# Performance work log

Hardware: AMD Instinct MI355X
Metric: run time of the kernel (lower is better)

## Reference

```python
import jax, jax.numpy as jnp
import numpy as np
import math

D = 256
H = 128
GATE_IN = 2 * D + 1 + 1 + 3  # mu, logvar, s, minutes, snr(3) = 517


def setup_inputs() -> dict:
    key = jax.random.key(0)
    ks = jax.random.split(key, 10)
    B, S = 256, 512
    mu = jax.random.normal(ks[0], (B, S, D), dtype=jnp.float32)
    logvar = jax.random.normal(ks[1], (B, S, D), dtype=jnp.float32)
    minutes = jax.random.uniform(ks[2], (B, S), dtype=jnp.float32) * 120.0
    mu_c = jax.random.normal(ks[3], (2, D), dtype=jnp.float32) * 0.1
    log_tau2 = jax.random.normal(ks[4], (2, D), dtype=jnp.float32) * 0.1
    log_prior = jax.random.normal(ks[5], (2,), dtype=jnp.float32) * 0.1
    W1 = jax.random.normal(ks[6], (H, GATE_IN), dtype=jnp.float32) * 0.05
    b1 = jnp.zeros((H,), dtype=jnp.float32)
    W2 = jax.random.normal(ks[7], (1, H), dtype=jnp.float32) * 0.05
    b2 = jnp.zeros((1,), dtype=jnp.float32)
    alpha_logits = jnp.float32(0.0)          # logit(0.5)
    attn_lambda_logit = jnp.float32(0.0)     # logit(0.5)
    decay_rate_log = jnp.float32(math.log(0.1))
    return dict(mu=mu, logvar=logvar, minutes=minutes, mu_c=mu_c,
                log_tau2=log_tau2, log_prior=log_prior, W1=W1, b1=b1,
                W2=W2, b2=b2, alpha_logits=alpha_logits,
                attn_lambda_logit=attn_lambda_logit,
                decay_rate_log=decay_rate_log)


def _logit(p):
    return jnp.log(p) - jnp.log1p(-p)


def reference(mu, logvar, minutes, mu_c, log_tau2, log_prior,
              W1, b1, W2, b2, alpha_logits, attn_lambda_logit,
              decay_rate_log):
    var = jnp.exp(logvar)                              # [B,S,D]

    def ell(c):
        tau2 = jnp.exp(log_tau2[c])                    # [D]
        diff2 = (mu - mu_c[c]) ** 2
        return -0.5 * jnp.sum((var + diff2) / tau2 + log_tau2[c], axis=-1)

    s = (ell(1) + log_prior[1]) - (ell(0) + log_prior[0])   # [B,S]

    # SNR features
    var_c = jnp.clip(var, 1e-6, None)
    snr1 = jnp.linalg.norm(mu, axis=-1) / math.sqrt(mu.shape[-1])
    snr2 = jnp.mean(logvar, axis=-1)
    snr3 = jnp.mean(mu ** 2 / var_c, axis=-1)
    snr = jnp.stack([snr1, snr2, snr3], axis=-1)            # [B,S,3]

    gate_in = jnp.concatenate(
        [mu, logvar, s[..., None], minutes[..., None], snr], axis=-1)

    h = jax.nn.relu(jnp.einsum('bsf,hf->bsh', gate_in, W1) + b1)
    a_raw = jax.nn.sigmoid(jnp.einsum('bsh,oh->bso', h, W2) + b2)[..., 0]

    # precision attention mixture
    score = jnp.sum(mu ** 2 / var_c, axis=-1)               # [B,S]
    a_prec = jax.nn.softmax(score, axis=1)
    a_mlp = a_raw / jnp.clip(jnp.sum(a_raw, axis=1, keepdims=True), 1e-6, None)
    lam = jax.nn.sigmoid(attn_lambda_logit)
    a = lam * a_mlp + (1.0 - lam) * a_prec

    # time decay
    last_time = jnp.max(minutes, axis=1, keepdims=True)
    delta_h = jnp.clip(last_time - minutes, 0.0, None) / 60.0
    rate = jax.nn.softplus(decay_rate_log)
    w = a * jnp.exp(-rate * delta_h)
    a = w / jnp.clip(jnp.sum(w, axis=1, keepdims=True), 1e-6, None)

    # mean aggregator
    s_main = jnp.sum(a * s, axis=1)                         # [B]

    # Noisy-OR branch
    p_i = jnp.clip(jax.nn.sigmoid(s) * a, 1e-6, 1.0 - 1e-6)
    log1m = jnp.sum(jnp.log1p(-p_i), axis=1)
    p_or = 1.0 - jnp.exp(log1m)
    s_or = _logit(jnp.clip(p_or, 1e-6, 1.0 - 1e-6))

    alpha = jax.nn.sigmoid(alpha_logits)
    s_total = alpha * s_main + (1.0 - alpha) * s_or
    return (s_total, s, a)
```

## Files before the change

### kernel.cpp

```cpp
#include <hip/hip_runtime.h>
#include <hip/hip_bf16.h>

#define B_DIM 256
#define NTOK (256 * 512)
#define W1_LD 517
#define TPB 32

#define WS_DIT 0
#define WS_E 256
#define WS_C0 512
#define WS_W1F 1024
#define WS_SCORE 36864

typedef __attribute__((ext_vector_type(8))) short bf16x8;
typedef __attribute__((ext_vector_type(4))) float f32x4;

__device__ __forceinline__ unsigned pk2(float a, float b) {
  __hip_bfloat162 h = __float22bfloat162_rn(make_float2(a, b));
  unsigned r;
  __builtin_memcpy(&r, &h, 4);
  return r;
}

template <int CTRL>
__device__ __forceinline__ float dpp_add(float v) {
  int s = __builtin_amdgcn_update_dpp(0, __float_as_int(v), CTRL, 0xf, 0xf,
                                      true);
  return v + __int_as_float(s);
}
__device__ __forceinline__ float row8_sum(float v) {
  v = dpp_add<0xB1>(v);
  v = dpp_add<0x4E>(v);
  v = dpp_add<0x141>(v);
  return v;
}
__device__ __forceinline__ float row16_sum(float v) {
  v = dpp_add<0xB1>(v);
  v = dpp_add<0x4E>(v);
  v = dpp_add<0x124>(v);
  v = dpp_add<0x128>(v);
  return v;
}

__device__ __forceinline__ float wave_sum(float v) {
#pragma unroll
  for (int off = 32; off > 0; off >>= 1) v += __shfl_xor(v, off, 64);
  return v;
}
__device__ __forceinline__ float wave_max(float v) {
#pragma unroll
  for (int off = 32; off > 0; off >>= 1) v = fmaxf(v, __shfl_xor(v, off, 64));
  return v;
}
__device__ __forceinline__ float block_sum(float v, float* scr) {
  v = wave_sum(v);
  int wid = threadIdx.x >> 6;
  __syncthreads();
  if ((threadIdx.x & 63) == 0) scr[wid] = v;
  __syncthreads();
  return scr[0] + scr[1] + scr[2] + scr[3];
}

__global__ __launch_bounds__(256) void k_setup(
    const float* __restrict__ W1, const float* __restrict__ b1,
    const float* __restrict__ mu_c, const float* __restrict__ log_tau2,
    const float* __restrict__ log_prior, float* __restrict__ wsc) {
  const int tid = threadIdx.x;
  const int h = blockIdx.x;
  ushort* w1f = (ushort*)(wsc + WS_W1F);
  const float* wr = W1 + h * W1_LD;
  const int k = 2 * tid;
  const unsigned pk = pk2(wr[k], wr[k + 1]);
  const int flat = (h >> 4) * 8704 + (k >> 5) * 512 +
                   (((k >> 3) & 3) * 16 + (h & 15)) * 8 + (k & 7);
  *(unsigned*)(w1f + flat) = pk;
  if (tid == 0) {
    const int base16 = (h >> 4) * 8704 + 16 * 512;
    uint4 g0;
    g0.x = pk2(wr[512], wr[513]);
    g0.y = pk2(wr[514], wr[515]);
    g0.z = pk2(wr[516], b1[h]);
    g0.w = 0u;
    *(uint4*)(w1f + base16 + ((h & 15)) * 8) = g0;
    const uint4 z = {0u, 0u, 0u, 0u};
    *(uint4*)(w1f + base16 + (16 + (h & 15)) * 8) = z;
    *(uint4*)(w1f + base16 + (32 + (h & 15)) * 8) = z;
    *(uint4*)(w1f + base16 + (48 + (h & 15)) * 8) = z;
  }

  if (blockIdx.x == 0) {
    __shared__ float scr[4];
    float lt0 = log_tau2[tid], lt1 = log_tau2[256 + tid];
    float mc0 = mu_c[tid], mc1 = mu_c[256 + tid];
    float it0 = __expf(-lt0), it1 = __expf(-lt1);
    wsc[WS_DIT + tid] = it1 - it0;
    wsc[WS_E + tid] = 2.0f * (mc1 * it1 - mc0 * it0);
    float g = mc1 * mc1 * it1 - mc0 * mc0 * it0 + (lt1 - lt0);
    float sg = block_sum(g, scr);
    if (tid == 0) wsc[WS_C0] = (log_prior[1] - log_prior[0]) - 0.5f * sg;
  }
}

__global__ __launch_bounds__(256, 4) void k_token(
    const float* __restrict__ mu, const float* __restrict__ logvar,
    const float* __restrict__ minutes, const float* __restrict__ W2g,
    const float* __restrict__ b2, const float* __restrict__ wsc,
    float* __restrict__ out_s, float* __restrict__ ws_score,
    float* __restrict__ araw_out) {
  __shared__ __align__(16) ushort A_l[TPB * 512];
  __shared__ __align__(16) ushort axl[TPB * 32];
  __shared__ float red2[4][TPB];

  const int tid = threadIdx.x;
  const int w = tid >> 6;
  const int l = tid & 63;
  const int tokbase = blockIdx.x * TPB;
  const float C0 = wsc[WS_C0];

  if (tid < 96) {
    const int row = tid & 31;
    const int c = tid >> 5;
    const uint4 z = {0u, 0u, 0u, 0u};
    *(uint4*)((char*)axl + row * 64 + 16 + c * 16) = z;
  }

  const int trow = tid >> 3;
  const int l8 = tid & 7;
  const int swz = (trow & 7) << 4;
  char* Ab = (char*)A_l;
  const size_t gbase = (size_t)(tokbase + trow) * 256 + l8 * 8;
  const float* ditg = wsc + WS_DIT + l8 * 8;
  const float* eg = wsc + WS_E + l8 * 8;
  float Ss = 0.f, Sm = 0.f, Sl = 0.f, Sc = 0.f;
#pragma unroll
  for (int t = 0; t < 4; ++t) {
    const float4 m0 = *(const float4*)(mu + gbase + t * 64);
    const float4 m1 = *(const float4*)(mu + gbase + t * 64 + 4);
    const float4 v0 = *(const float4*)(logvar + gbase + t * 64);
    const float4 v1 = *(const float4*)(logvar + gbase + t * 64 + 4);
    const float4 dA = *(const float4*)(ditg + t * 64);
    const float4 dB = *(const float4*)(ditg + t * 64 + 4);
    const float4 eA = *(const float4*)(eg + t * 64);
    const float4 eB = *(const float4*)(eg + t * 64 + 4);
#define CHUNK(m, lv, dt, ee)                                              \
  {                                                                       \
    const float va = __expf(lv.x), vb = __expf(lv.y), vc = __expf(lv.z),  \
                vd = __expf(lv.w);                                        \
    const float na = __expf(-lv.x), nb = __expf(-lv.y),                   \
                nc = __expf(-lv.z), nd = __expf(-lv.w);                   \
    const float qa = m.x * m.x, qb = m.y * m.y, qc = m.z * m.z,           \
                qd = m.w * m.w;                                           \
    Ss += (va + qa) * dt.x - m.x * ee.x + (vb + qb) * dt.y - m.y * ee.y + \
          (vc + qc) * dt.z - m.z * ee.z + (vd + qd) * dt.w - m.w * ee.w;  \
    Sm += qa + qb + qc + qd;                                              \
    Sl += lv.x + lv.y + lv.z + lv.w;                                      \
    Sc += qa * na + qb * nb + qc * nc + qd * nd;                          \
  }
    CHUNK(m0, v0, dA, eA);
    CHUNK(m1, v1, dB, eB);
#undef CHUNK
    uint4 um, uv;
    um.x = pk2(m0.x, m0.y);
    um.y = pk2(m0.z, m0.w);
    um.z = pk2(m1.x, m1.y);
    um.w = pk2(m1.z, m1.w);
    uv.x = pk2(v0.x, v0.y);
    uv.y = pk2(v0.z, v0.w);
    uv.z = pk2(v1.x, v1.y);
    uv.w = pk2(v1.z, v1.w);
    const int off = trow * 1024 + t * 128 + l8 * 16;
    *(uint4*)(Ab + (off ^ swz)) = um;
    *(uint4*)(Ab + ((off + 512) ^ swz)) = uv;
  }
  Ss = row8_sum(Ss);
  Sm = row8_sum(Sm);
  Sl = row8_sum(Sl);
  Sc = row8_sum(Sc);
  if (l8 == 0) {
    const float sval = -0.5f * Ss + C0;
    const float mn = minutes[tokbase + trow];
    uint4 ex;
    ex.x = pk2(sval, mn);
    ex.y = pk2(sqrtf(Sm) * (1.0f / 16.0f), Sl * (1.0f / 256.0f));
    ex.z = pk2(Sc * (1.0f / 256.0f), 1.0f);
    ex.w = 0u;
    *(uint4*)((char*)axl + trow * 64) = ex;
    out_s[tokbase + trow] = sval;
    ws_score[tokbase + trow] = Sc;
  }
  __syncthreads();

  f32x4 a00 = {0.f, 0.f, 0.f, 0.f};
  f32x4 a01 = {0.f, 0.f, 0.f, 0.f};
  f32x4 a10 = {0.f, 0.f, 0.f, 0.f};
  f32x4 a11 = {0.f, 0.f, 0.f, 0.f};
  const int m_lane = l & 15;
  const int swzA = (m_lane & 7) << 4;
  const int rowA0 = m_lane * 1024;
  const int rowA1 = rowA0 + 16 * 1024;
  const ushort* w1f = (const ushort*)(wsc + WS_W1F);
  const ushort* bp0 = w1f + (2 * w) * 8704 + l * 8;
  const ushort* bp1 = bp0 + 8704;
#pragma unroll 4
  for (int ks = 0; ks < 16; ++ks) {
    const int kByte = ks * 64 + (l >> 4) * 16;
    bf16x8 f0 = *(const bf16x8*)(Ab + ((rowA0 + kByte) ^ swzA));
    bf16x8 f1 = *(const bf16x8*)(Ab + ((rowA1 + kByte) ^ swzA));
    bf16x8 bq0 = *(const bf16x8*)(bp0 + ks * 512);
    bf16x8 bq1 = *(const bf16x8*)(bp1 + ks * 512);
    a00 = __builtin_amdgcn_mfma_f32_16x16x32_bf16(f0, bq0, a00, 0, 0, 0);
    a01 = __builtin_amdgcn_mfma_f32_16x16x32_bf16(f0, bq1, a01, 0, 0, 0);
    a10 = __builtin_amdgcn_mfma_f32_16x16x32_bf16(f1, bq0, a10, 0, 0, 0);
    a11 = __builtin_amdgcn_mfma_f32_16x16x32_bf16(f1, bq1, a11, 0, 0, 0);
  }
  {
    const int xb = (l >> 4) * 16;
    bf16x8 f0 = *(const bf16x8*)((char*)axl + m_lane * 64 + xb);
    bf16x8 f1 = *(const bf16x8*)((char*)axl + (m_lane + 16) * 64 + xb);
    bf16x8 bq0 = *(const bf16x8*)(bp0 + 16 * 512);
    bf16x8 bq1 = *(const bf16x8*)(bp1 + 16 * 512);
    a00 = __builtin_amdgcn_mfma_f32_16x16x32_bf16(f0, bq0, a00, 0, 0, 0);
    a01 = __builtin_amdgcn_mfma_f32_16x16x32_bf16(f0, bq1, a01, 0, 0, 0);
    a10 = __builtin_amdgcn_mfma_f32_16x16x32_bf16(f1, bq0, a10, 0, 0, 0);
    a11 = __builtin_amdgcn_mfma_f32_16x16x32_bf16(f1, bq1, a11, 0, 0, 0);
  }

  const int g = l >> 4;
  const float w2a = W2g[32 * w + m_lane];
  const float w2b = W2g[32 * w + m_lane + 16];
#pragma unroll
  for (int mf = 0; mf < 2; ++mf) {
    const f32x4 aN0 = mf ? a10 : a00;
    const f32x4 aN1 = mf ? a11 : a01;
#pragma unroll
    for (int r = 0; r < 4; ++r) {
      const int t_loc = 16 * mf + 4 * g + r;
      float cs = fmaxf(aN0[r], 0.f) * w2a + fmaxf(aN1[r], 0.f) * w2b;
      cs = row16_sum(cs);
      if (m_lane == 0) red2[w][t_loc] = cs;
    }
  }
  __syncthreads();
  if (tid < TPB) {
    float z = red2[0][tid] + red2[1][tid] + red2[2][tid] + red2[3][tid] +
              b2[0];
    araw_out[tokbase + tid] = 1.0f / (1.0f + __expf(-z));
  }
}

__global__ __launch_bounds__(256) void k_row(
    const float* __restrict__ minutes, const float* __restrict__ s_in,
    const float* __restrict__ score_in, float* a_io,
    const float* __restrict__ alpha_logits,
    const float* __restrict__ attn_lambda_logit,
    const float* __restrict__ decay_rate_log, float* __restrict__ out_total) {
  __shared__ float scrA[4][4];
  __shared__ float scrB[4];
  __shared__ float scrC[4];
  __shared__ float scrD[4][2];
  const int row = blockIdx.x;
  const int tid = threadIdx.x;
  const int w = tid >> 6;
  const int base = row * 512;
  const float sc0 = score_in[base + tid], sc1 = score_in[base + 256 + tid];
  const float sv0 = s_in[base + tid], sv1 = s_in[base + 256 + tid];
  const float ar0 = a_io[base + tid], ar1 = a_io[base + 256 + tid];
  const float mn0 = minutes[base + tid], mn1 = minutes[base + 256 + tid];

  const float vsc = wave_max(fmaxf(sc0, sc1));
  const float vmn = wave_max(fmaxf(mn0, mn1));
  const float var_ = wave_sum(ar0 + ar1);
  if ((tid & 63) == 0) {
    scrA[w][0] = vsc;
    scrA[w][1] = vmn;
    scrA[w][2] = var_;
  }
  __syncthreads();
  const float msc = fmaxf(fmaxf(scrA[0][0], scrA[1][0]),
                          fmaxf(scrA[2][0], scrA[3][0]));
  const float mmn = fmaxf(fmaxf(scrA[0][1], scrA[1][1]),
                          fmaxf(scrA[2][1], scrA[3][1]));
  const float sar = scrA[0][2] + scrA[1][2] + scrA[2][2] + scrA[3][2];

  const float e0 = __expf(sc0 - msc), e1 = __expf(sc1 - msc);
  const float vse = wave_sum(e0 + e1);
  if ((tid & 63) == 0) scrB[w] = vse;
  __syncthreads();
  const float se = scrB[0] + scrB[1] + scrB[2] + scrB[3];

  const float lam = 1.0f / (1.0f + __expf(-attn_lambda_logit[0]));
  const float alpha = 1.0f / (1.0f + __expf(-alpha_logits[0]));
  const float rate = log1pf(__expf(decay_rate_log[0]));

  const float inv_sar = 1.0f / fmaxf(sar, 1e-6f);
  const float inv_se = 1.0f / se;
  const float a00 = lam * ar0 * inv_sar + (1.0f - lam) * e0 * inv_se;
  const float a01 = lam * ar1 * inv_sar + (1.0f - lam) * e1 * inv_se;
  const float dh0 = fmaxf(mmn - mn0, 0.0f) * (1.0f / 60.0f);
  const float dh1 = fmaxf(mmn - mn1, 0.0f) * (1.0f / 60.0f);
  const float w0 = a00 * __expf(-rate * dh0);
  const float w1 = a01 * __expf(-rate * dh1);
  const float vsw = wave_sum(w0 + w1);
  if ((tid & 63) == 0) scrC[w] = vsw;
  __syncthreads();
  const float sw = scrC[0] + scrC[1] + scrC[2] + scrC[3];
  const float inv_sw = 1.0f / fmaxf(sw, 1e-6f);
  const float af0 = w0 * inv_sw, af1 = w1 * inv_sw;
  a_io[base + tid] = af0;
  a_io[base + 256 + tid] = af1;

  const float sg0 = 1.0f / (1.0f + __expf(-sv0));
  const float sg1 = 1.0f / (1.0f + __expf(-sv1));
  const float p0 = fminf(fmaxf(sg0 * af0, 1e-6f), 1.0f - 1e-6f);
  const float p1 = fminf(fmaxf(sg1 * af1, 1e-6f), 1.0f - 1e-6f);
  const float vsm = wave_sum(af0 * sv0 + af1 * sv1);
  const float vlg = wave_sum(log1pf(-p0) + log1pf(-p1));
  if ((tid & 63) == 0) {
    scrD[w][0] = vsm;
    scrD[w][1] = vlg;
  }
  __syncthreads();
  if (tid == 0) {
    const float smain = scrD[0][0] + scrD[1][0] + scrD[2][0] + scrD[3][0];
    const float slg = scrD[0][1] + scrD[1][1] + scrD[2][1] + scrD[3][1];
    float por = 1.0f - __expf(slg);
    por = fminf(fmaxf(por, 1e-6f), 1.0f - 1e-6f);
    const float sor = logf(por) - log1pf(-por);
    out_total[row] = alpha * smain + (1.0f - alpha) * sor;
  }
}

extern "C" void kernel_launch(void* const* d_in, const int* in_sizes, int n_in,
                              void* d_out, int out_size, void* d_ws,
                              size_t ws_size, hipStream_t stream) {
  const float* mu = (const float*)d_in[0];
  const float* logvar = (const float*)d_in[1];
  const float* minutes = (const float*)d_in[2];
  const float* mu_c = (const float*)d_in[3];
  const float* log_tau2 = (const float*)d_in[4];
  const float* log_prior = (const float*)d_in[5];
  const float* W1 = (const float*)d_in[6];
  const float* b1 = (const float*)d_in[7];
  const float* W2 = (const float*)d_in[8];
  const float* b2 = (const float*)d_in[9];
  const float* alpha_logits = (const float*)d_in[10];
  const float* attn_lambda_logit = (const float*)d_in[11];
  const float* decay_rate_log = (const float*)d_in[12];

  float* out = (float*)d_out;
  float* out_total = out;
  float* out_s = out + B_DIM;
  float* out_a = out + B_DIM + NTOK;
  float* wsc = (float*)d_ws;
  float* ws_score = wsc + WS_SCORE;

  k_setup<<<128, 256, 0, stream>>>(W1, b1, mu_c, log_tau2, log_prior, wsc);
  k_token<<<NTOK / TPB, 256, 0, stream>>>(mu, logvar, minutes, W2, b2, wsc,
                                          out_s, ws_score, out_a);
  k_row<<<B_DIM, 256, 0, stream>>>(minutes, out_s, ws_score, out_a,
                                   alpha_logits, attn_lambda_logit,
                                   decay_rate_log, out_total);
}
```

Baseline: 69.04 us.

## Switch gate MLP first layer from bf16 to fp8 MFMA with repacked weights

```diff
diff --git a/kernel.cpp b/kernel.cpp
--- a/kernel.cpp
+++ b/kernel.cpp
@@ -10,16 +10,23 @@
 #define WS_E 256
 #define WS_C0 512
 #define WS_W1F 1024
-#define WS_SCORE 36864
+#define WS_W1X 17408
+#define WS_SCORE 20480
 
 typedef __attribute__((ext_vector_type(8))) short bf16x8;
 typedef __attribute__((ext_vector_type(4))) float f32x4;
+typedef long long i64;
 
 __device__ __forceinline__ unsigned pk2(float a, float b) {
   __hip_bfloat162 h = __float22bfloat162_rn(make_float2(a, b));
   unsigned r;
   __builtin_memcpy(&r, &h, 4);
   return r;
+}
+__device__ __forceinline__ unsigned pk4f8(float a, float b, float c, float d) {
+  int r = __builtin_amdgcn_cvt_pk_fp8_f32(a, b, 0, false);
+  r = __builtin_amdgcn_cvt_pk_fp8_f32(c, d, r, true);
+  return (unsigned)r;
 }
 
 template <int CTRL>
@@ -67,25 +74,33 @@
     const float* __restrict__ log_prior, float* __restrict__ wsc) {
   const int tid = threadIdx.x;
   const int h = blockIdx.x;
-  ushort* w1f = (ushort*)(wsc + WS_W1F);
   const float* wr = W1 + h * W1_LD;
-  const int k = 2 * tid;
-  const unsigned pk = pk2(wr[k], wr[k + 1]);
-  const int flat = (h >> 4) * 8704 + (k >> 5) * 512 +
-                   (((k >> 3) & 3) * 16 + (h & 15)) * 8 + (k & 7);
-  *(unsigned*)(w1f + flat) = pk;
+  {
+    const int p = 2 * tid;
+    const int c0 = ((p & 15) < 8) ? (p >> 4) * 8 + (p & 7)
+                                  : 256 + (p >> 4) * 8 + (p & 7);
+    const int p1 = p + 1;
+    const int c1 = ((p1 & 15) < 8) ? (p1 >> 4) * 8 + (p1 & 7)
+                                   : 256 + (p1 >> 4) * 8 + (p1 & 7);
+    const int pk = __builtin_amdgcn_cvt_pk_fp8_f32(wr[c0], wr[c1], 0, false);
+    char* w1f = (char*)(wsc + WS_W1F);
+    const int off = (h >> 4) * 8192 + (p >> 5) * 512 +
+                    (((p >> 3) & 3) * 16 + (h & 15)) * 8 + (p & 7);
+    *(ushort*)(w1f + off) = (ushort)pk;
+  }
   if (tid == 0) {
-    const int base16 = (h >> 4) * 8704 + 16 * 512;
+    ushort* w1x = (ushort*)(wsc + WS_W1X);
+    const int nb = (h >> 4) * 512;
     uint4 g0;
     g0.x = pk2(wr[512], wr[513]);
     g0.y = pk2(wr[514], wr[515]);
     g0.z = pk2(wr[516], b1[h]);
     g0.w = 0u;
-    *(uint4*)(w1f + base16 + ((h & 15)) * 8) = g0;
+    *(uint4*)(w1x + nb + (h & 15) * 8) = g0;
     const uint4 z = {0u, 0u, 0u, 0u};
-    *(uint4*)(w1f + base16 + (16 + (h & 15)) * 8) = z;
-    *(uint4*)(w1f + base16 + (32 + (h & 15)) * 8) = z;
-    *(uint4*)(w1f + base16 + (48 + (h & 15)) * 8) = z;
+    *(uint4*)(w1x + nb + (16 + (h & 15)) * 8) = z;
+    *(uint4*)(w1x + nb + (32 + (h & 15)) * 8) = z;
+    *(uint4*)(w1x + nb + (48 + (h & 15)) * 8) = z;
   }
 
   if (blockIdx.x == 0) {
@@ -101,13 +116,13 @@
   }
 }
 
-__global__ __launch_bounds__(256, 4) void k_token(
+__global__ __launch_bounds__(256, 8) void k_token(
     const float* __restrict__ mu, const float* __restrict__ logvar,
     const float* __restrict__ minutes, const float* __restrict__ W2g,
     const float* __restrict__ b2, const float* __restrict__ wsc,
     float* __restrict__ out_s, float* __restrict__ ws_score,
     float* __restrict__ araw_out) {
-  __shared__ __align__(16) ushort A_l[TPB * 512];
+  __shared__ __align__(16) char A_l[TPB * 512];
   __shared__ __align__(16) ushort axl[TPB * 32];
   __shared__ float red2[4][TPB];
 
@@ -127,7 +142,6 @@
   const int trow = tid >> 3;
   const int l8 = tid & 7;
   const int swz = (trow & 7) << 4;
-  char* Ab = (char*)A_l;
   const size_t gbase = (size_t)(tokbase + trow) * 256 + l8 * 8;
   const float* ditg = wsc + WS_DIT + l8 * 8;
   const float* eg = wsc + WS_E + l8 * 8;
@@ -159,18 +173,13 @@
     CHUNK(m0, v0, dA, eA);
     CHUNK(m1, v1, dB, eB);
 #undef CHUNK
-    uint4 um, uv;
-    um.x = pk2(m0.x, m0.y);
-    um.y = pk2(m0.z, m0.w);
-    um.z = pk2(m1.x, m1.y);
-    um.w = pk2(m1.z, m1.w);
-    uv.x = pk2(v0.x, v0.y);
-    uv.y = pk2(v0.z, v0.w);
-    uv.z = pk2(v1.x, v1.y);
-    uv.w = pk2(v1.z, v1.w);
-    const int off = trow * 1024 + t * 128 + l8 * 16;
-    *(uint4*)(Ab + (off ^ swz)) = um;
-    *(uint4*)(Ab + ((off + 512) ^ swz)) = uv;
+    uint4 u;
+    u.x = pk4f8(m0.x, m0.y, m0.z, m0.w);
+    u.y = pk4f8(m1.x, m1.y, m1.z, m1.w);
+    u.z = pk4f8(v0.x, v0.y, v0.z, v0.w);
+    u.w = pk4f8(v1.x, v1.y, v1.z, v1.w);
+    const int col = trow * 512 + (t * 8 + l8) * 16;
+    *(uint4*)(A_l + (col ^ swz)) = u;
   }
   Ss = row8_sum(Ss);
   Sm = row8_sum(Sm);
@@ -196,29 +205,30 @@
   f32x4 a11 = {0.f, 0.f, 0.f, 0.f};
   const int m_lane = l & 15;
   const int swzA = (m_lane & 7) << 4;
-  const int rowA0 = m_lane * 1024;
-  const int rowA1 = rowA0 + 16 * 1024;
-  const ushort* w1f = (const ushort*)(wsc + WS_W1F);
-  const ushort* bp0 = w1f + (2 * w) * 8704 + l * 8;
-  const ushort* bp1 = bp0 + 8704;
+  const int rowA0 = m_lane * 512;
+  const int rowA1 = rowA0 + 16 * 512;
+  const char* w1f = (const char*)(wsc + WS_W1F);
+  const char* bp0 = w1f + (2 * w) * 8192 + l * 8;
+  const char* bp1 = bp0 + 8192;
 #pragma unroll 4
   for (int ks = 0; ks < 16; ++ks) {
-    const int kByte = ks * 64 + (l >> 4) * 16;
-    bf16x8 f0 = *(const bf16x8*)(Ab + ((rowA0 + kByte) ^ swzA));
-    bf16x8 f1 = *(const bf16x8*)(Ab + ((rowA1 + kByte) ^ swzA));
-    bf16x8 bq0 = *(const bf16x8*)(bp0 + ks * 512);
-    bf16x8 bq1 = *(const bf16x8*)(bp1 + ks * 512);
-    a00 = __builtin_amdgcn_mfma_f32_16x16x32_bf16(f0, bq0, a00, 0, 0, 0);
-    a01 = __builtin_amdgcn_mfma_f32_16x16x32_bf16(f0, bq1, a01, 0, 0, 0);
-    a10 = __builtin_amdgcn_mfma_f32_16x16x32_bf16(f1, bq0, a10, 0, 0, 0);
-    a11 = __builtin_amdgcn_mfma_f32_16x16x32_bf16(f1, bq1, a11, 0, 0, 0);
+    const int kOff = ks * 32 + (l >> 4) * 8;
+    i64 f0 = *(const i64*)(A_l + ((rowA0 + kOff) ^ swzA));
+    i64 f1 = *(const i64*)(A_l + ((rowA1 + kOff) ^ swzA));
+    i64 bq0 = *(const i64*)(bp0 + ks * 512);
+    i64 bq1 = *(const i64*)(bp1 + ks * 512);
+    a00 = __builtin_amdgcn_mfma_f32_16x16x32_fp8_fp8(f0, bq0, a00, 0, 0, 0);
+    a01 = __builtin_amdgcn_mfma_f32_16x16x32_fp8_fp8(f0, bq1, a01, 0, 0, 0);
+    a10 = __builtin_amdgcn_mfma_f32_16x16x32_fp8_fp8(f1, bq0, a10, 0, 0, 0);
+    a11 = __builtin_amdgcn_mfma_f32_16x16x32_fp8_fp8(f1, bq1, a11, 0, 0, 0);
   }
   {
     const int xb = (l >> 4) * 16;
     bf16x8 f0 = *(const bf16x8*)((char*)axl + m_lane * 64 + xb);
     bf16x8 f1 = *(const bf16x8*)((char*)axl + (m_lane + 16) * 64 + xb);
-    bf16x8 bq0 = *(const bf16x8*)(bp0 + 16 * 512);
-    bf16x8 bq1 = *(const bf16x8*)(bp1 + 16 * 512);
+    const ushort* w1x = (const ushort*)(wsc + WS_W1X);
+    bf16x8 bq0 = *(const bf16x8*)(w1x + (2 * w) * 512 + l * 8);
+    bf16x8 bq1 = *(const bf16x8*)(w1x + (2 * w + 1) * 512 + l * 8);
     a00 = __builtin_amdgcn_mfma_f32_16x16x32_bf16(f0, bq0, a00, 0, 0, 0);
     a01 = __builtin_amdgcn_mfma_f32_16x16x32_bf16(f0, bq1, a01, 0, 0, 0);
     a10 = __builtin_amdgcn_mfma_f32_16x16x32_bf16(f1, bq0, a10, 0, 0, 0);
```

Result: faster. 58.31 us (-15.5%).
